# Kernel optimization log

Measured on AMD Instinct MI355X. Metric: run time of the kernel, lower is better.

## Reference

```python
import jax, jax.numpy as jnp
import numpy as np

D = 128
SCALE = 1.0 / np.sqrt(D)  # scalar_value


def setup_inputs() -> dict:
    key = jax.random.key(0)
    k1, k2, k3 = jax.random.split(key, 3)
    B, N, S = 2, 16, 2048
    q = jax.random.normal(k1, (B, N, S, D), dtype=jnp.float32)
    k = jax.random.normal(k2, (B, N, S, D), dtype=jnp.float32)
    v = jax.random.normal(k3, (B, N, S, D), dtype=jnp.float32)
    return {"q": q, "k": k, "v": v}


def reference(q, k, v):
    # BNSD layout. scores = scale * Q K^T, causal mask, softmax with
    # explicit max/sum tracking (golden for NPU fusion attention).
    s1, s2 = q.shape[2], k.shape[2]
    scores = jnp.einsum('bnsd,bntd->bnst', q, k) * SCALE
    # generate_attn_mask: causal (lower-triangular kept), masked -> -inf
    causal = jnp.triu(jnp.ones((s1, s2), dtype=bool), k=1)
    scores = jnp.where(causal, -jnp.inf, scores)
    softmax_max = jnp.max(scores, axis=-1, keepdims=True)          # [B,N,S,1]
    exp_scores = jnp.exp(scores - softmax_max)
    softmax_sum = jnp.sum(exp_scores, axis=-1, keepdims=True)      # [B,N,S,1]
    softmax_res = exp_scores / softmax_sum
    out = jnp.einsum('bnst,bntd->bnsd', softmax_res, v)
    # NPU golden repeats stats x8 along last dim
    return (out,
            jnp.tile(softmax_max, (1, 1, 1, 8)),
            jnp.tile(softmax_sum, (1, 1, 1, 8)))
```

## Files before the change

### kernel.cpp

```cpp
#include <hip/hip_runtime.h>
#include <math.h>
#include <stdint.h>

#define D_DIM 128
#define SEQ 2048
#define NHEADS 32
#define BC 64
#define SCALE 0.08838834764831843f

typedef short bf16x8 __attribute__((ext_vector_type(8)));
typedef float f32x4 __attribute__((ext_vector_type(4)));

union Frag { uint32_t u[4]; bf16x8 v; unsigned short s[8]; };
union Pack8 { unsigned short s[8]; uint4 q; };

__device__ __forceinline__ uint32_t fbits(float x) { return __builtin_bit_cast(uint32_t, x); }
__device__ __forceinline__ float bbits(uint32_t u) { return __builtin_bit_cast(float, u); }
__device__ __forceinline__ unsigned short bf16_rne(float x) {
    uint32_t u = fbits(x);
    u += 0x7FFFu + ((u >> 16) & 1u);
    return (unsigned short)(u >> 16);
}
__device__ __forceinline__ void split2(float a, float b, uint32_t& hp, uint32_t& lp) {
    uint32_t ua = fbits(a) & 0xFFFF0000u, ub = fbits(b) & 0xFFFF0000u;
    float la = a - bbits(ua), lb = b - bbits(ub);
    hp = (ua >> 16) | ub;
    lp = (fbits(la) >> 16) | (fbits(lb) & 0xFFFF0000u);
}

__global__ __launch_bounds__(512, 2) void fa_fused(
    const float* __restrict__ q, const float* __restrict__ k,
    const float* __restrict__ v, float* __restrict__ out)
{
    __shared__ __align__(16) unsigned short KhsB[2][64 * 128];
    __shared__ __align__(16) unsigned short KlsB[2][64 * 128];
    __shared__ __align__(16) unsigned short VhsB[2][128 * 64];
    __shared__ __align__(16) unsigned short Pbs[128 * 64];

    const int x  = blockIdx.x;
    const int xi = x >> 5;
    const int h  = x & 31;

    const int t    = (int)threadIdx.x;
    const int wb   = t >> 6;
    const int lane = t & 63;
    const int ln   = lane & 15;
    const int qd   = lane >> 4;

    const float* qh = q + (size_t)h * SEQ * D_DIM;
    const float* kh = k + (size_t)h * SEQ * D_DIM;
    const float* vh = v + (size_t)h * SEQ * D_DIM;
    float* out_o = out;
    float* out_m = out + (size_t)NHEADS * SEQ * D_DIM;
    float* out_l = out_m + (size_t)NHEADS * SEQ * 8;

    const int krow0 = t >> 5;
    const int kd4   = t & 31;
    const int vcc   = wb;
    const int vd0   = lane;

    for (int ph = 0; ph < 2; ++ph) {
        const int it = ph ? xi : (15 - xi);
        const int qrow0 = it * 128 + wb * 16;

        Frag Qh[4], Ql[4];
        {
            const float* qp = qh + (size_t)(qrow0 + ln) * D_DIM;
            #pragma unroll
            for (int kc = 0; kc < 4; ++kc) {
                const int kb = kc * 32 + qd * 8;
                float e[8];
                *(float4*)(e)     = *(const float4*)(qp + kb);
                *(float4*)(e + 4) = *(const float4*)(qp + kb + 4);
                #pragma unroll
                for (int j = 0; j < 8; ++j) e[j] *= SCALE;
                #pragma unroll
                for (int j = 0; j < 4; ++j)
                    split2(e[2 * j], e[2 * j + 1], Qh[kc].u[j], Ql[kc].u[j]);
            }
        }

        float4 kreg[4];
        float  vraw[2][8];
        uint2  khi[4], klo[4];
        uint4  vcv[2];

        #pragma unroll
        for (int itr = 0; itr < 4; ++itr)
            kreg[itr] = *(const float4*)(kh + (size_t)(itr * 16 + krow0) * D_DIM + kd4 * 4);
        #pragma unroll
        for (int uu = 0; uu < 2; ++uu) {
            const int d = uu * 64 + vd0;
            #pragma unroll
            for (int j = 0; j < 8; ++j)
                vraw[uu][j] = vh[(size_t)(vcc * 8 + j) * D_DIM + d];
        }
        #pragma unroll
        for (int itr = 0; itr < 4; ++itr) {
            uint32_t hp0, lp0, hp1, lp1;
            split2(kreg[itr].x, kreg[itr].y, hp0, lp0);
            split2(kreg[itr].z, kreg[itr].w, hp1, lp1);
            khi[itr] = make_uint2(hp0, hp1);
            klo[itr] = make_uint2(lp0, lp1);
        }
        #pragma unroll
        for (int uu = 0; uu < 2; ++uu) {
            Pack8 p8;
            #pragma unroll
            for (int j = 0; j < 8; ++j) p8.s[j] = bf16_rne(vraw[uu][j]);
            vcv[uu] = p8.q;
        }
        {
            unsigned short* Kh0 = KhsB[0];
            unsigned short* Kl0 = KlsB[0];
            unsigned short* Vh0 = VhsB[0];
            #pragma unroll
            for (int itr = 0; itr < 4; ++itr) {
                const int row = itr * 16 + krow0;
                const int off = row * 128 + (((kd4 >> 1) ^ (row & 7)) * 8) + (kd4 & 1) * 4;
                *(uint2*)(Kh0 + off) = khi[itr];
                *(uint2*)(Kl0 + off) = klo[itr];
            }
            #pragma unroll
            for (int uu = 0; uu < 2; ++uu) {
                const int d = uu * 64 + vd0;
                *(uint4*)(Vh0 + d * 64 + ((vcc ^ (d & 7)) * 8)) = vcv[uu];
            }
        }
        __syncthreads();

        f32x4 accO[8];
        float m_r[4], l_r[4];
        #pragma unroll
        for (int nd = 0; nd < 8; ++nd) accO[nd] = (f32x4){0.f, 0.f, 0.f, 0.f};
        #pragma unroll
        for (int r = 0; r < 4; ++r) { m_r[r] = -INFINITY; l_r[r] = 0.f; }

        const int jt_end = 2 * it + 1;
        for (int jt = 0; jt <= jt_end; ++jt) {
            const int c0  = jt * BC;
            const int cur = jt & 1;

            if (jt < jt_end) {
                const int c0n = c0 + BC;
                const float* kp2 = kh + (size_t)c0n * D_DIM;
                #pragma unroll
                for (int itr = 0; itr < 4; ++itr)
                    kreg[itr] = *(const float4*)(kp2 + (size_t)(itr * 16 + krow0) * D_DIM + kd4 * 4);
                #pragma unroll
                for (int uu = 0; uu < 2; ++uu) {
                    const int d = uu * 64 + vd0;
                    #pragma unroll
                    for (int j = 0; j < 8; ++j)
                        vraw[uu][j] = vh[(size_t)(c0n + vcc * 8 + j) * D_DIM + d];
                }
            }

            if (c0 <= qrow0 + 15) {
                const unsigned short* Khs = KhsB[cur];
                const unsigned short* Kls = KlsB[cur];
                const unsigned short* Vhs = VhsB[cur];
                f32x4 accS[4];
                #pragma unroll
                for (int nt = 0; nt < 4; ++nt) accS[nt] = (f32x4){0.f, 0.f, 0.f, 0.f};
                #pragma unroll
                for (int kc = 0; kc < 4; ++kc) {
                    #pragma unroll
                    for (int nt = 0; nt < 4; ++nt) {
                        int n = nt * 16 + ln;
                        int off = n * 128 + (((kc * 4 + qd) ^ (n & 7)) * 8);
                        Frag Bh, Bl;
                        Bh.v = *(const bf16x8*)(Khs + off);
                        Bl.v = *(const bf16x8*)(Kls + off);
                        f32x4 c = accS[nt];
                        c = __builtin_amdgcn_mfma_f32_16x16x32_bf16(Qh[kc].v, Bh.v, c, 0, 0, 0);
                        c = __builtin_amdgcn_mfma_f32_16x16x32_bf16(Qh[kc].v, Bl.v, c, 0, 0, 0);
                        c = __builtin_amdgcn_mfma_f32_16x16x32_bf16(Ql[kc].v, Bh.v, c, 0, 0, 0);
                        accS[nt] = c;
                    }
                }
                const bool needMask = (c0 + 63 > qrow0);
                float mxr[4];
                #pragma unroll
                for (int r = 0; r < 4; ++r) {
                    const int rowg = qrow0 + qd * 4 + r;
                    float mx = -INFINITY;
                    #pragma unroll
                    for (int nt = 0; nt < 4; ++nt) {
                        float s = accS[nt][r];
                        if (needMask && (c0 + nt * 16 + ln > rowg)) s = -INFINITY;
                        accS[nt][r] = s;
                        mx = fmaxf(mx, s);
                    }
                    mxr[r] = mx;
                }
                #pragma unroll
                for (int r = 0; r < 4; ++r) {
                    #pragma unroll
                    for (int off = 1; off < 16; off <<= 1) mxr[r] = fmaxf(mxr[r], __shfl_xor(mxr[r], off));
                }
                const bool grow = (mxr[0] > m_r[0]) | (mxr[1] > m_r[1]) |
                                  (mxr[2] > m_r[2]) | (mxr[3] > m_r[3]);
                if (__any(grow)) {
                    #pragma unroll
                    for (int r = 0; r < 4; ++r) {
                        const float mnew = fmaxf(m_r[r], mxr[r]);
                        const float alpha = __expf(m_r[r] - mnew);
                        m_r[r] = mnew;
                        l_r[r] *= alpha;
                        #pragma unroll
                        for (int nd = 0; nd < 8; ++nd) accO[nd][r] *= alpha;
                    }
                }
                #pragma unroll
                for (int r = 0; r < 4; ++r) {
                    float p[4];
                    #pragma unroll
                    for (int nt = 0; nt < 4; ++nt) p[nt] = __expf(accS[nt][r] - m_r[r]);
                    l_r[r] += (p[0] + p[1]) + (p[2] + p[3]);
                    const int R = wb * 16 + qd * 4 + r;
                    #pragma unroll
                    for (int nt = 0; nt < 4; ++nt) {
                        int c = nt * 16 + ln;
                        Pbs[R * 64 + (((c >> 3) ^ (R & 7)) * 8) + (c & 7)] = bf16_rne(p[nt]);
                    }
                }
                #pragma unroll
                for (int kc2 = 0; kc2 < 2; ++kc2) {
                    Frag Pf;
                    const int R = wb * 16 + ln;
                    Pf.v = *(const bf16x8*)(Pbs + R * 64 + (((kc2 * 4 + qd) ^ (R & 7)) * 8));
                    #pragma unroll
                    for (int nd = 0; nd < 8; ++nd) {
                        int dcol = nd * 16 + ln;
                        int voff = dcol * 64 + (((kc2 * 4 + qd) ^ (dcol & 7)) * 8);
                        Frag Vh2;
                        Vh2.v = *(const bf16x8*)(Vhs + voff);
                        accO[nd] = __builtin_amdgcn_mfma_f32_16x16x32_bf16(Pf.v, Vh2.v, accO[nd], 0, 0, 0);
                    }
                }
            }

            if (jt < jt_end) {
                #pragma unroll
                for (int itr = 0; itr < 4; ++itr) {
                    uint32_t hp0, lp0, hp1, lp1;
                    split2(kreg[itr].x, kreg[itr].y, hp0, lp0);
                    split2(kreg[itr].z, kreg[itr].w, hp1, lp1);
                    khi[itr] = make_uint2(hp0, hp1);
                    klo[itr] = make_uint2(lp0, lp1);
                }
                #pragma unroll
                for (int uu = 0; uu < 2; ++uu) {
                    Pack8 p8;
                    #pragma unroll
                    for (int j = 0; j < 8; ++j) p8.s[j] = bf16_rne(vraw[uu][j]);
                    vcv[uu] = p8.q;
                }
                unsigned short* Khn = KhsB[cur ^ 1];
                unsigned short* Kln = KlsB[cur ^ 1];
                unsigned short* Vhn = VhsB[cur ^ 1];
                #pragma unroll
                for (int itr = 0; itr < 4; ++itr) {
                    const int row = itr * 16 + krow0;
                    const int off = row * 128 + (((kd4 >> 1) ^ (row & 7)) * 8) + (kd4 & 1) * 4;
                    *(uint2*)(Khn + off) = khi[itr];
                    *(uint2*)(Kln + off) = klo[itr];
                }
                #pragma unroll
                for (int uu = 0; uu < 2; ++uu) {
                    const int d = uu * 64 + vd0;
                    *(uint4*)(Vhn + d * 64 + ((vcc ^ (d & 7)) * 8)) = vcv[uu];
                }
            }

            __syncthreads();
        }

        #pragma unroll
        for (int r = 0; r < 4; ++r) {
            #pragma unroll
            for (int off = 1; off < 16; off <<= 1) l_r[r] += __shfl_xor(l_r[r], off);
        }
        #pragma unroll
        for (int r = 0; r < 4; ++r) {
            const int rowg = qrow0 + qd * 4 + r;
            const float invl = 1.0f / l_r[r];
            float* op = out_o + (size_t)h * SEQ * D_DIM + (size_t)rowg * D_DIM;
            #pragma unroll
            for (int nd = 0; nd < 8; ++nd) op[nd * 16 + ln] = accO[nd][r] * invl;
            if (ln < 8) {
                size_t sb = ((size_t)h * SEQ + rowg) * 8 + ln;
                out_m[sb] = m_r[r];
                out_l[sb] = l_r[r];
            }
        }
    }
}

extern "C" void kernel_launch(void* const* d_in, const int* in_sizes, int n_in,
                              void* d_out, int out_size, void* d_ws, size_t ws_size,
                              hipStream_t stream) {
    const float* q = (const float*)d_in[0];
    const float* k = (const float*)d_in[1];
    const float* v = (const float*)d_in[2];
    float* out = (float*)d_out;
    (void)d_ws; (void)ws_size;

    fa_fused<<<dim3(256), dim3(512), 0, stream>>>(q, k, v, out);
}
```

Baseline: 227.1 us.

## Process both causal q-tiles concurrently in one 1024-thread block sharing K/V tiles

Each block previously handled its paired heavy and light query tiles one after another with 512 threads, loading K/V twice. Now 16 waves split into two groups, one per query tile, and they share a single K/V load loop that runs over the heavy tile's range. This halves K/V global loads and staging work per block and removes the serial second phase. The cost is larger blocks, so lower occupancy per CU. The light group also sits idle through the later iterations while still taking part in every barrier.

```diff
diff --git a/kernel.cpp b/kernel.cpp
--- a/kernel.cpp
+++ b/kernel.cpp
@@ -28,14 +28,14 @@
     lp = (fbits(la) >> 16) | (fbits(lb) & 0xFFFF0000u);
 }
 
-__global__ __launch_bounds__(512, 2) void fa_fused(
+__global__ __launch_bounds__(1024) void fa_fused(
     const float* __restrict__ q, const float* __restrict__ k,
     const float* __restrict__ v, float* __restrict__ out)
 {
     __shared__ __align__(16) unsigned short KhsB[2][64 * 128];
     __shared__ __align__(16) unsigned short KlsB[2][64 * 128];
     __shared__ __align__(16) unsigned short VhsB[2][128 * 64];
-    __shared__ __align__(16) unsigned short Pbs[128 * 64];
+    __shared__ __align__(16) unsigned short Pbs[256 * 64];
 
     const int x  = blockIdx.x;
     const int xi = x >> 5;
@@ -46,6 +46,11 @@
     const int lane = t & 63;
     const int ln   = lane & 15;
     const int qd   = lane >> 4;
+    const int grp  = wb >> 3;
+    const int wbl  = wb & 7;
+
+    const int it    = grp ? xi : (15 - xi);
+    const int qrow0 = it * 128 + wbl * 16;
 
     const float* qh = q + (size_t)h * SEQ * D_DIM;
     const float* kh = k + (size_t)h * SEQ * D_DIM;
@@ -56,244 +61,221 @@
 
     const int krow0 = t >> 5;
     const int kd4   = t & 31;
-    const int vcc   = wb;
-    const int vd0   = lane;
-
-    for (int ph = 0; ph < 2; ++ph) {
-        const int it = ph ? xi : (15 - xi);
-        const int qrow0 = it * 128 + wb * 16;
-
-        Frag Qh[4], Ql[4];
-        {
-            const float* qp = qh + (size_t)(qrow0 + ln) * D_DIM;
+    const int vcc   = wb >> 1;
+    const int vd    = (wb & 1) * 64 + lane;
+
+    Frag Qh[4], Ql[4];
+    {
+        const float* qp = qh + (size_t)(qrow0 + ln) * D_DIM;
+        #pragma unroll
+        for (int kc = 0; kc < 4; ++kc) {
+            const int kb = kc * 32 + qd * 8;
+            float e[8];
+            *(float4*)(e)     = *(const float4*)(qp + kb);
+            *(float4*)(e + 4) = *(const float4*)(qp + kb + 4);
+            #pragma unroll
+            for (int j = 0; j < 8; ++j) e[j] *= SCALE;
+            #pragma unroll
+            for (int j = 0; j < 4; ++j)
+                split2(e[2 * j], e[2 * j + 1], Qh[kc].u[j], Ql[kc].u[j]);
+        }
+    }
+
+    float4 kreg[2];
+    float  vraw[8];
+    uint2  khi[2], klo[2];
+    uint4  vcv;
+
+    #pragma unroll
+    for (int i = 0; i < 2; ++i)
+        kreg[i] = *(const float4*)(kh + (size_t)(i * 32 + krow0) * D_DIM + kd4 * 4);
+    #pragma unroll
+    for (int j = 0; j < 8; ++j)
+        vraw[j] = vh[(size_t)(vcc * 8 + j) * D_DIM + vd];
+    #pragma unroll
+    for (int i = 0; i < 2; ++i) {
+        uint32_t hp0, lp0, hp1, lp1;
+        split2(kreg[i].x, kreg[i].y, hp0, lp0);
+        split2(kreg[i].z, kreg[i].w, hp1, lp1);
+        khi[i] = make_uint2(hp0, hp1);
+        klo[i] = make_uint2(lp0, lp1);
+    }
+    {
+        Pack8 p8;
+        #pragma unroll
+        for (int j = 0; j < 8; ++j) p8.s[j] = bf16_rne(vraw[j]);
+        vcv = p8.q;
+    }
+    {
+        unsigned short* Kh0 = KhsB[0];
+        unsigned short* Kl0 = KlsB[0];
+        unsigned short* Vh0 = VhsB[0];
+        #pragma unroll
+        for (int i = 0; i < 2; ++i) {
+            const int row = i * 32 + krow0;
+            const int off = row * 128 + (((kd4 >> 1) ^ (row & 7)) * 8) + (kd4 & 1) * 4;
+            *(uint2*)(Kh0 + off) = khi[i];
+            *(uint2*)(Kl0 + off) = klo[i];
+        }
+        *(uint4*)(Vh0 + vd * 64 + ((vcc ^ (vd & 7)) * 8)) = vcv;
+    }
+    __syncthreads();
+
+    f32x4 accO[8];
+    float m_r[4], l_r[4];
+    #pragma unroll
+    for (int nd = 0; nd < 8; ++nd) accO[nd] = (f32x4){0.f, 0.f, 0.f, 0.f};
+    #pragma unroll
+    for (int r = 0; r < 4; ++r) { m_r[r] = -INFINITY; l_r[r] = 0.f; }
+
+    const int jt_end = 2 * (15 - xi) + 1;
+    for (int jt = 0; jt <= jt_end; ++jt) {
+        const int c0  = jt * BC;
+        const int cur = jt & 1;
+
+        if (jt < jt_end) {
+            const int c0n = c0 + BC;
+            const float* kp2 = kh + (size_t)c0n * D_DIM;
+            #pragma unroll
+            for (int i = 0; i < 2; ++i)
+                kreg[i] = *(const float4*)(kp2 + (size_t)(i * 32 + krow0) * D_DIM + kd4 * 4);
+            #pragma unroll
+            for (int j = 0; j < 8; ++j)
+                vraw[j] = vh[(size_t)(c0n + vcc * 8 + j) * D_DIM + vd];
+        }
+
+        if (c0 <= qrow0 + 15) {
+            const unsigned short* Khs = KhsB[cur];
+            const unsigned short* Kls = KlsB[cur];
+            const unsigned short* Vhs = VhsB[cur];
+            f32x4 accS[4];
+            #pragma unroll
+            for (int nt = 0; nt < 4; ++nt) accS[nt] = (f32x4){0.f, 0.f, 0.f, 0.f};
             #pragma unroll
             for (int kc = 0; kc < 4; ++kc) {
-                const int kb = kc * 32 + qd * 8;
-                float e[8];
-                *(float4*)(e)     = *(const float4*)(qp + kb);
-                *(float4*)(e + 4) = *(const float4*)(qp + kb + 4);
-                #pragma unroll
-                for (int j = 0; j < 8; ++j) e[j] *= SCALE;
-                #pragma unroll
-                for (int j = 0; j < 4; ++j)
-                    split2(e[2 * j], e[2 * j + 1], Qh[kc].u[j], Ql[kc].u[j]);
-            }
-        }
-
-        float4 kreg[4];
-        float  vraw[2][8];
-        uint2  khi[4], klo[4];
-        uint4  vcv[2];
-
-        #pragma unroll
-        for (int itr = 0; itr < 4; ++itr)
-            kreg[itr] = *(const float4*)(kh + (size_t)(itr * 16 + krow0) * D_DIM + kd4 * 4);
-        #pragma unroll
-        for (int uu = 0; uu < 2; ++uu) {
-            const int d = uu * 64 + vd0;
-            #pragma unroll
-            for (int j = 0; j < 8; ++j)
-                vraw[uu][j] = vh[(size_t)(vcc * 8 + j) * D_DIM + d];
-        }
-        #pragma unroll
-        for (int itr = 0; itr < 4; ++itr) {
-            uint32_t hp0, lp0, hp1, lp1;
-            split2(kreg[itr].x, kreg[itr].y, hp0, lp0);
-            split2(kreg[itr].z, kreg[itr].w, hp1, lp1);
-            khi[itr] = make_uint2(hp0, hp1);
-            klo[itr] = make_uint2(lp0, lp1);
-        }
-        #pragma unroll
-        for (int uu = 0; uu < 2; ++uu) {
-            Pack8 p8;
-            #pragma unroll
-            for (int j = 0; j < 8; ++j) p8.s[j] = bf16_rne(vraw[uu][j]);
-            vcv[uu] = p8.q;
-        }
-        {
-            unsigned short* Kh0 = KhsB[0];
-            unsigned short* Kl0 = KlsB[0];
-            unsigned short* Vh0 = VhsB[0];
-            #pragma unroll
-            for (int itr = 0; itr < 4; ++itr) {
-                const int row = itr * 16 + krow0;
+                #pragma unroll
+                for (int nt = 0; nt < 4; ++nt) {
+                    int n = nt * 16 + ln;
+                    int off = n * 128 + (((kc * 4 + qd) ^ (n & 7)) * 8);
+                    Frag Bh, Bl;
+                    Bh.v = *(const bf16x8*)(Khs + off);
+                    Bl.v = *(const bf16x8*)(Kls + off);
+                    f32x4 c = accS[nt];
+                    c = __builtin_amdgcn_mfma_f32_16x16x32_bf16(Qh[kc].v, Bh.v, c, 0, 0, 0);
+                    c = __builtin_amdgcn_mfma_f32_16x16x32_bf16(Qh[kc].v, Bl.v, c, 0, 0, 0);
+                    c = __builtin_amdgcn_mfma_f32_16x16x32_bf16(Ql[kc].v, Bh.v, c, 0, 0, 0);
+                    accS[nt] = c;
+                }
+            }
+            const bool needMask = (c0 + 63 > qrow0);
+            float mxr[4];
+            #pragma unroll
+            for (int r = 0; r < 4; ++r) {
+                const int rowg = qrow0 + qd * 4 + r;
+                float mx = -INFINITY;
+                #pragma unroll
+                for (int nt = 0; nt < 4; ++nt) {
+                    float s = accS[nt][r];
+                    if (needMask && (c0 + nt * 16 + ln > rowg)) s = -INFINITY;
+                    accS[nt][r] = s;
+                    mx = fmaxf(mx, s);
+                }
+                mxr[r] = mx;
+            }
+            #pragma unroll
+            for (int r = 0; r < 4; ++r) {
+                #pragma unroll
+                for (int off = 1; off < 16; off <<= 1) mxr[r] = fmaxf(mxr[r], __shfl_xor(mxr[r], off));
+            }
+            const bool grow = (mxr[0] > m_r[0]) | (mxr[1] > m_r[1]) |
+                              (mxr[2] > m_r[2]) | (mxr[3] > m_r[3]);
+            if (__any(grow)) {
+                #pragma unroll
+                for (int r = 0; r < 4; ++r) {
+                    const float mnew = fmaxf(m_r[r], mxr[r]);
+                    const float alpha = __expf(m_r[r] - mnew);
+                    m_r[r] = mnew;
+                    l_r[r] *= alpha;
+                    #pragma unroll
+                    for (int nd = 0; nd < 8; ++nd) accO[nd][r] *= alpha;
+                }
+            }
+            #pragma unroll
+            for (int r = 0; r < 4; ++r) {
+                float p[4];
+                #pragma unroll
+                for (int nt = 0; nt < 4; ++nt) p[nt] = __expf(accS[nt][r] - m_r[r]);
+                l_r[r] += (p[0] + p[1]) + (p[2] + p[3]);
+                const int R = wb * 16 + qd * 4 + r;
+                #pragma unroll
+                for (int nt = 0; nt < 4; ++nt) {
+                    int c = nt * 16 + ln;
+                    Pbs[R * 64 + (((c >> 3) ^ (R & 7)) * 8) + (c & 7)] = bf16_rne(p[nt]);
+                }
+            }
+            #pragma unroll
+            for (int kc2 = 0; kc2 < 2; ++kc2) {
+                Frag Pf;
+                const int R = wb * 16 + ln;
+                Pf.v = *(const bf16x8*)(Pbs + R * 64 + (((kc2 * 4 + qd) ^ (R & 7)) * 8));
+                #pragma unroll
+                for (int nd = 0; nd < 8; ++nd) {
+                    int dcol = nd * 16 + ln;
+                    int voff = dcol * 64 + (((kc2 * 4 + qd) ^ (dcol & 7)) * 8);
+                    Frag Vh2;
+                    Vh2.v = *(const bf16x8*)(Vhs + voff);
+                    accO[nd] = __builtin_amdgcn_mfma_f32_16x16x32_bf16(Pf.v, Vh2.v, accO[nd], 0, 0, 0);
+                }
+            }
+        }
+
+        if (jt < jt_end) {
+            #pragma unroll
+            for (int i = 0; i < 2; ++i) {
+                uint32_t hp0, lp0, hp1, lp1;
+                split2(kreg[i].x, kreg[i].y, hp0, lp0);
+                split2(kreg[i].z, kreg[i].w, hp1, lp1);
+                khi[i] = make_uint2(hp0, hp1);
+                klo[i] = make_uint2(lp0, lp1);
+            }
+            {
+                Pack8 p8;
+                #pragma unroll
+                for (int j = 0; j < 8; ++j) p8.s[j] = bf16_rne(vraw[j]);
+                vcv = p8.q;
+            }
+            unsigned short* Khn = KhsB[cur ^ 1];
+            unsigned short* Kln = KlsB[cur ^ 1];
+            unsigned short* Vhn = VhsB[cur ^ 1];
+            #pragma unroll
+            for (int i = 0; i < 2; ++i) {
+                const int row = i * 32 + krow0;
                 const int off = row * 128 + (((kd4 >> 1) ^ (row & 7)) * 8) + (kd4 & 1) * 4;
-                *(uint2*)(Kh0 + off) = khi[itr];
-                *(uint2*)(Kl0 + off) = klo[itr];
-            }
-            #pragma unroll
-            for (int uu = 0; uu < 2; ++uu) {
-                const int d = uu * 64 + vd0;
-                *(uint4*)(Vh0 + d * 64 + ((vcc ^ (d & 7)) * 8)) = vcv[uu];
-            }
-        }
+                *(uint2*)(Khn + off) = khi[i];
+                *(uint2*)(Kln + off) = klo[i];
+            }
+            *(uint4*)(Vhn + vd * 64 + ((vcc ^ (vd & 7)) * 8)) = vcv;
+        }
+
         __syncthreads();
-
-        f32x4 accO[8];
-        float m_r[4], l_r[4];
-        #pragma unroll
-        for (int nd = 0; nd < 8; ++nd) accO[nd] = (f32x4){0.f, 0.f, 0.f, 0.f};
-        #pragma unroll
-        for (int r = 0; r < 4; ++r) { m_r[r] = -INFINITY; l_r[r] = 0.f; }
-
-        const int jt_end = 2 * it + 1;
-        for (int jt = 0; jt <= jt_end; ++jt) {
-            const int c0  = jt * BC;
-            const int cur = jt & 1;
-
-            if (jt < jt_end) {
-                const int c0n = c0 + BC;
-                const float* kp2 = kh + (size_t)c0n * D_DIM;
-                #pragma unroll
-                for (int itr = 0; itr < 4; ++itr)
-                    kreg[itr] = *(const float4*)(kp2 + (size_t)(itr * 16 + krow0) * D_DIM + kd4 * 4);
-                #pragma unroll
-                for (int uu = 0; uu < 2; ++uu) {
-                    const int d = uu * 64 + vd0;
-                    #pragma unroll
-                    for (int j = 0; j < 8; ++j)
-                        vraw[uu][j] = vh[(size_t)(c0n + vcc * 8 + j) * D_DIM + d];
-                }
-            }
-
-            if (c0 <= qrow0 + 15) {
-                const unsigned short* Khs = KhsB[cur];
-                const unsigned short* Kls = KlsB[cur];
-                const unsigned short* Vhs = VhsB[cur];
-                f32x4 accS[4];
-                #pragma unroll
-                for (int nt = 0; nt < 4; ++nt) accS[nt] = (f32x4){0.f, 0.f, 0.f, 0.f};
-                #pragma unroll
-                for (int kc = 0; kc < 4; ++kc) {
-                    #pragma unroll
-                    for (int nt = 0; nt < 4; ++nt) {
-                        int n = nt * 16 + ln;
-                        int off = n * 128 + (((kc * 4 + qd) ^ (n & 7)) * 8);
-                        Frag Bh, Bl;
-                        Bh.v = *(const bf16x8*)(Khs + off);
-                        Bl.v = *(const bf16x8*)(Kls + off);
-                        f32x4 c = accS[nt];
-                        c = __builtin_amdgcn_mfma_f32_16x16x32_bf16(Qh[kc].v, Bh.v, c, 0, 0, 0);
-                        c = __builtin_amdgcn_mfma_f32_16x16x32_bf16(Qh[kc].v, Bl.v, c, 0, 0, 0);
-                        c = __builtin_amdgcn_mfma_f32_16x16x32_bf16(Ql[kc].v, Bh.v, c, 0, 0, 0);
-                        accS[nt] = c;
-                    }
-                }
-                const bool needMask = (c0 + 63 > qrow0);
-                float mxr[4];
-                #pragma unroll
-                for (int r = 0; r < 4; ++r) {
-                    const int rowg = qrow0 + qd * 4 + r;
-                    float mx = -INFINITY;
-                    #pragma unroll
-                    for (int nt = 0; nt < 4; ++nt) {
-                        float s = accS[nt][r];
-                        if (needMask && (c0 + nt * 16 + ln > rowg)) s = -INFINITY;
-                        accS[nt][r] = s;
-                        mx = fmaxf(mx, s);
-                    }
-                    mxr[r] = mx;
-                }
-                #pragma unroll
-                for (int r = 0; r < 4; ++r) {
-                    #pragma unroll
-                    for (int off = 1; off < 16; off <<= 1) mxr[r] = fmaxf(mxr[r], __shfl_xor(mxr[r], off));
-                }
-                const bool grow = (mxr[0] > m_r[0]) | (mxr[1] > m_r[1]) |
-                                  (mxr[2] > m_r[2]) | (mxr[3] > m_r[3]);
-                if (__any(grow)) {
-                    #pragma unroll
-                    for (int r = 0; r < 4; ++r) {
-                        const float mnew = fmaxf(m_r[r], mxr[r]);
-                        const float alpha = __expf(m_r[r] - mnew);
-                        m_r[r] = mnew;
-                        l_r[r] *= alpha;
-                        #pragma unroll
-                        for (int nd = 0; nd < 8; ++nd) accO[nd][r] *= alpha;
-                    }
-                }
-                #pragma unroll
-                for (int r = 0; r < 4; ++r) {
-                    float p[4];
-                    #pragma unroll
-                    for (int nt = 0; nt < 4; ++nt) p[nt] = __expf(accS[nt][r] - m_r[r]);
-                    l_r[r] += (p[0] + p[1]) + (p[2] + p[3]);
-                    const int R = wb * 16 + qd * 4 + r;
-                    #pragma unroll
-                    for (int nt = 0; nt < 4; ++nt) {
-                        int c = nt * 16 + ln;
-                        Pbs[R * 64 + (((c >> 3) ^ (R & 7)) * 8) + (c & 7)] = bf16_rne(p[nt]);
-                    }
-                }
-                #pragma unroll
-                for (int kc2 = 0; kc2 < 2; ++kc2) {
-                    Frag Pf;
-                    const int R = wb * 16 + ln;
-                    Pf.v = *(const bf16x8*)(Pbs + R * 64 + (((kc2 * 4 + qd) ^ (R & 7)) * 8));
-                    #pragma unroll
-                    for (int nd = 0; nd < 8; ++nd) {
-                        int dcol = nd * 16 + ln;
-                        int voff = dcol * 64 + (((kc2 * 4 + qd) ^ (dcol & 7)) * 8);
-                        Frag Vh2;
-                        Vh2.v = *(const bf16x8*)(Vhs + voff);
-                        accO[nd] = __builtin_amdgcn_mfma_f32_16x16x32_bf16(Pf.v, Vh2.v, accO[nd], 0, 0, 0);
-                    }
-                }
-            }
-
-            if (jt < jt_end) {
-                #pragma unroll
-                for (int itr = 0; itr < 4; ++itr) {
-                    uint32_t hp0, lp0, hp1, lp1;
-                    split2(kreg[itr].x, kreg[itr].y, hp0, lp0);
-                    split2(kreg[itr].z, kreg[itr].w, hp1, lp1);
-                    khi[itr] = make_uint2(hp0, hp1);
-                    klo[itr] = make_uint2(lp0, lp1);
-                }
-                #pragma unroll
-                for (int uu = 0; uu < 2; ++uu) {
-                    Pack8 p8;
-                    #pragma unroll
-                    for (int j = 0; j < 8; ++j) p8.s[j] = bf16_rne(vraw[uu][j]);
-                    vcv[uu] = p8.q;
-                }
-                unsigned short* Khn = KhsB[cur ^ 1];
-                unsigned short* Kln = KlsB[cur ^ 1];
-                unsigned short* Vhn = VhsB[cur ^ 1];
-                #pragma unroll
-                for (int itr = 0; itr < 4; ++itr) {
-                    const int row = itr * 16 + krow0;
-                    const int off = row * 128 + (((kd4 >> 1) ^ (row & 7)) * 8) + (kd4 & 1) * 4;
-                    *(uint2*)(Khn + off) = khi[itr];
-                    *(uint2*)(Kln + off) = klo[itr];
-                }
-                #pragma unroll
-                for (int uu = 0; uu < 2; ++uu) {
-                    const int d = uu * 64 + vd0;
-                    *(uint4*)(Vhn + d * 64 + ((vcc ^ (d & 7)) * 8)) = vcv[uu];
-                }
-            }
-
-            __syncthreads();
-        }
-
-        #pragma unroll
-        for (int r = 0; r < 4; ++r) {
-            #pragma unroll
-            for (int off = 1; off < 16; off <<= 1) l_r[r] += __shfl_xor(l_r[r], off);
-        }
-        #pragma unroll
-        for (int r = 0; r < 4; ++r) {
-            const int rowg = qrow0 + qd * 4 + r;
-            const float invl = 1.0f / l_r[r];
-            float* op = out_o + (size_t)h * SEQ * D_DIM + (size_t)rowg * D_DIM;
-            #pragma unroll
-            for (int nd = 0; nd < 8; ++nd) op[nd * 16 + ln] = accO[nd][r] * invl;
-            if (ln < 8) {
-                size_t sb = ((size_t)h * SEQ + rowg) * 8 + ln;
-                out_m[sb] = m_r[r];
-                out_l[sb] = l_r[r];
-            }
+    }
+
+    #pragma unroll
+    for (int r = 0; r < 4; ++r) {
+        #pragma unroll
+        for (int off = 1; off < 16; off <<= 1) l_r[r] += __shfl_xor(l_r[r], off);
+    }
+    #pragma unroll
+    for (int r = 0; r < 4; ++r) {
+        const int rowg = qrow0 + qd * 4 + r;
+        const float invl = 1.0f / l_r[r];
+        float* op = out_o + (size_t)h * SEQ * D_DIM + (size_t)rowg * D_DIM;
+        #pragma unroll
+        for (int nd = 0; nd < 8; ++nd) op[nd * 16 + ln] = accO[nd][r] * invl;
+        if (ln < 8) {
+            size_t sb = ((size_t)h * SEQ + rowg) * 8 + ln;
+            out_m[sb] = m_r[r];
+            out_l[sb] = l_r[r];
         }
     }
 }
@@ -307,5 +289,5 @@
     float* out = (float*)d_out;
     (void)d_ws; (void)ws_size;
 
-    fa_fused<<<dim3(256), dim3(512), 0, stream>>>(q, k, v, out);
-}
+    fa_fused<<<dim3(256), dim3(1024), 0, stream>>>(q, k, v, out);
+}
```

Result: slower. 387.4 us (+70.6%).
